# Kernel tuning notes

Measured on AMD Instinct MI355X. Metric: run time of the kernel, lower is better.

The kernel has to match this reference:

```python
import jax, jax.numpy as jnp
import numpy as np

N_NODES = 100000
N_EDGES = 3200000
N_GRAPHS = 512
F_IN = 128
HID = 256
N_LABELS = 10


def setup_inputs() -> dict:
    key = jax.random.key(0)
    ks = jax.random.split(key, 16)
    x = jax.random.normal(ks[0], (N_NODES, F_IN), dtype=jnp.float32)
    edge_index = jax.random.randint(ks[1], (2, N_EDGES), 0, N_NODES)
    batch = jnp.sort(jax.random.randint(ks[2], (N_NODES,), 0, N_GRAPHS))
    dims = [(F_IN, HID), (HID, HID), (HID, HID), (HID, HID // 2), (HID // 2, HID // 2), (HID // 2, HID // 4)]
    inp = {"x": x, "edge_index": edge_index, "batch": batch, "primary_idxs_in_batch": 0}
    for i, (di, do) in enumerate(dims, 1):
        inp[f"W{i}"] = jax.random.normal(ks[2 + i], (di, do), dtype=jnp.float32) * (1.0 / np.sqrt(di))
        inp[f"b{i}"] = jnp.zeros((do,), dtype=jnp.float32)
    inp["Wlin"] = jax.random.normal(ks[12], (HID // 4, N_LABELS), dtype=jnp.float32) * (1.0 / np.sqrt(HID // 4))
    inp["blin"] = jnp.zeros((N_LABELS,), dtype=jnp.float32)
    return inp


def _gcn_conv(h, W, b, src, dst, norm):
    # dense transform first (smaller of the two sides), then normalized scatter-aggregate
    m = (h @ W)[src] * norm[:, None]  # [E+N, C_out]
    return jax.ops.segment_sum(m, dst, num_segments=N_NODES) + b


def reference(x, edge_index, batch, primary_idxs_in_batch,
              W1, b1, W2, b2, W3, b3, W4, b4, W5, b5, W6, b6, Wlin, blin):
    loops = jnp.arange(N_NODES, dtype=edge_index.dtype)
    src = jnp.concatenate([edge_index[0], loops])  # A + I (self loops)
    dst = jnp.concatenate([edge_index[1], loops])
    deg = jax.ops.segment_sum(jnp.ones_like(dst, dtype=x.dtype), dst, num_segments=N_NODES)
    dinv = jnp.where(deg > 0, jax.lax.rsqrt(deg), 0.0)
    norm = dinv[src] * dinv[dst]  # D^-1/2 (A+I) D^-1/2 edge weights

    h = jax.nn.relu(_gcn_conv(x, W1, b1, src, dst, norm))
    h = jax.nn.relu(_gcn_conv(h, W2, b2, src, dst, norm))
    h = jax.nn.relu(_gcn_conv(h, W3, b3, src, dst, norm))
    h = jax.nn.relu(_gcn_conv(h, W4, b4, src, dst, norm))
    h = jax.nn.relu(_gcn_conv(h, W5, b5, src, dst, norm))
    h = _gcn_conv(h, W6, b6, src, dst, norm)

    # primary_idxs_in_batch is falsy (0) -> global_mean_pool path
    s = jax.ops.segment_sum(h, batch, num_segments=N_GRAPHS)
    cnt = jax.ops.segment_sum(jnp.ones((N_NODES,), dtype=h.dtype), batch, num_segments=N_GRAPHS)
    pooled = s / jnp.maximum(cnt, 1.0)[:, None]  # [G, HID//4]

    logits = pooled @ Wlin + blin  # [G, labels]
    return (jax.nn.log_softmax(logits, axis=1), jax.nn.softmax(logits, axis=1))
```

## Files before the change

kernel.cpp:

```cpp
#include <hip/hip_runtime.h>
#include <math.h>

#define NN 100000
#define NE 3200000
#define NG 512
#define NBK 782
#define EBLK 196
#define SBE 16384
#define STSH 13
#define NTIL 13

typedef __attribute__((ext_vector_type(8))) short short8;
typedef __attribute__((ext_vector_type(4))) float f32x4;
typedef __attribute__((ext_vector_type(2))) float f32x2;

__device__ __forceinline__ float bf2f(unsigned short h){
  return __uint_as_float(((unsigned int)h) << 16);
}
__device__ __forceinline__ unsigned short f2bf(float f){
  unsigned int u = __float_as_uint(f);
  unsigned int r = (u + 0x7fffu + ((u >> 16) & 1u)) >> 16;
  return (unsigned short)r;
}
__device__ __forceinline__ unsigned char f2fp8(float v){
  int p = __builtin_amdgcn_cvt_pk_fp8_f32(v, v, 0, 0);
  return (unsigned char)p;
}

__global__ __launch_bounds__(256) void hist2_k(const int* __restrict__ ei,
    int* __restrict__ cnt, int* __restrict__ btot){
  __shared__ int lh[NBK];
  int t = threadIdx.x, b = blockIdx.x;
  for (int i=t; i<NBK; i+=256) lh[i] = 0;
  __syncthreads();
  int base = b*SBE;
  #pragma unroll 8
  for (int u=0; u<SBE/256; u++){
    int e = base + u*256 + t;
    if (e < NE) atomicAdd(&lh[ei[NE + e] >> 7], 1);
  }
  __syncthreads();
  for (int i=t; i<NBK; i+=256){
    int v = lh[i];
    cnt[b*NBK + i] = v;
    if (v) atomicAdd(&btot[i], v);
  }
}
__global__ void bscan2_k(const int* __restrict__ btot, int* __restrict__ bptr){
  __shared__ int sc[1024];
  int t = threadIdx.x;
  int v = (t < NBK) ? btot[t] : 0;
  sc[t] = v; __syncthreads();
  for (int off=1; off<1024; off<<=1){
    int u = (t>=off) ? sc[t-off] : 0;
    __syncthreads(); sc[t] += u; __syncthreads();
  }
  if (t < NBK) bptr[t] = sc[t] - v;
  if (t == 1023) bptr[NBK] = sc[1023];
}
__global__ __launch_bounds__(256) void bkpfx_k(int* __restrict__ cnt, const int* __restrict__ bptr){
  __shared__ int sc[256];
  int b = blockIdx.x, t = threadIdx.x;
  int v = (t < EBLK) ? cnt[t*NBK + b] : 0;
  sc[t] = v; __syncthreads();
  for (int off=1; off<256; off<<=1){
    int u = (t>=off) ? sc[t-off] : 0;
    __syncthreads(); sc[t] += u; __syncthreads();
  }
  if (t < EBLK) cnt[t*NBK + b] = bptr[b] + sc[t] - v;
}
__global__ __launch_bounds__(256) void scat2_k(const int* __restrict__ ei,
    const int* __restrict__ cnt, unsigned int* __restrict__ ebuf){
  __shared__ int lh[NBK];
  __shared__ int lo[NBK];
  int t = threadIdx.x, b = blockIdx.x;
  for (int i=t; i<NBK; i+=256){ lh[i] = 0; lo[i] = cnt[b*NBK + i]; }
  __syncthreads();
  int base = b*SBE;
  #pragma unroll 8
  for (int u=0; u<SBE/256; u++){
    int e = base + u*256 + t;
    if (e < NE){
      int s = ei[e], d = ei[NE + e];
      int bk = d >> 7;
      int r = atomicAdd(&lh[bk], 1);
      ebuf[lo[bk] + r] = (unsigned)s | ((unsigned)(d & 127) << 17);
    }
  }
}
__global__ __launch_bounds__(256) void bcsr_k(const unsigned int* __restrict__ ebuf,
    const int* __restrict__ bptr, int* __restrict__ rp, float* __restrict__ dinv,
    int* __restrict__ col, int* __restrict__ permg){
  __shared__ int cnt2[128*NTIL];
  __shared__ int sc[128];
  __shared__ int dg[128];
  int b = blockIdx.x, t = threadIdx.x;
  int nbase = b << 7;
  int beg = bptr[b], end = bptr[b+1];
  for (int i = t; i < 128*NTIL; i += 256) cnt2[i] = 0;
  __syncthreads();
  for (int e = beg + t; e < end; e += 256){
    unsigned int sd = ebuf[e];
    int li = sd >> 17;
    int tile = (int)(sd & 0x1FFFFu) >> STSH;
    atomicAdd(&cnt2[li*NTIL + tile], 1);
  }
  __syncthreads();
  int v = 0;
  if (t < 128){
    #pragma unroll
    for (int k=0;k<NTIL;k++) v += cnt2[t*NTIL+k];
    sc[t] = v;
    dg[t] = ((nbase + t) < NN) ? v : 0x7FFFFFFF;
  }
  __syncthreads();
  for (int o2=1; o2<128; o2<<=1){
    int u = (t < 128 && t >= o2) ? sc[t-o2] : 0;
    __syncthreads();
    if (t < 128) sc[t] += u;
    __syncthreads();
  }
  if (t < 128){
    int node = nbase + t;
    int ex = beg + sc[t] - v;
    if (node < NN){
      rp[node] = ex;
      dinv[node] = rsqrtf((float)(v + 1));
    }
    int s = ex;
    #pragma unroll
    for (int k=0;k<NTIL;k++){
      int c = cnt2[t*NTIL+k];
      cnt2[t*NTIL+k] = s;
      s += c;
    }
    int d = dg[t];
    int rk = 0;
    #pragma unroll 4
    for (int u2=0; u2<128; u2++){
      int du = dg[u2];
      rk += (int)((du < d) || (du == d && u2 < t));
    }
    permg[nbase + rk] = node;
  }
  if (b == ((NN-1) >> 7) && t == 0) rp[NN] = end;
  __syncthreads();
  for (int e = beg + t; e < end; e += 256){
    unsigned int sd = ebuf[e];
    int li = sd >> 17;
    int src = (int)(sd & 0x1FFFF);
    int tile = src >> STSH;
    int pos = atomicAdd(&cnt2[li*NTIL + tile], 1);
    col[pos] = src;
  }
}

__global__ void f2q_k(const float* __restrict__ in, unsigned char* __restrict__ out, int n4){
  int i = blockIdx.x*256 + threadIdx.x;
  if (i < n4){
    float4 v = ((const float4*)in)[i];
    int p = __builtin_amdgcn_cvt_pk_fp8_f32(v.x, v.y, 0, 0);
    p = __builtin_amdgcn_cvt_pk_fp8_f32(v.z, v.w, p, 1);
    ((unsigned int*)out)[i] = (unsigned int)p;
  }
}
__global__ void wswz_all_k(const float* W1, const float* W2, const float* W3,
                           const float* W4, const float* W5, const float* W6,
                           unsigned short* O1, unsigned short* O2, unsigned short* O3,
                           unsigned short* O4, unsigned short* O5, unsigned short* O6){
  int cfg = blockIdx.y;
  int K, N; const float* W; unsigned short* out;
  switch(cfg){
    case 0: K=128; N=256; W=W1; out=O1; break;
    case 1: K=256; N=256; W=W2; out=O2; break;
    case 2: K=256; N=256; W=W3; out=O3; break;
    case 3: K=256; N=128; W=W4; out=O4; break;
    case 4: K=128; N=128; W=W5; out=O5; break;
    default:K=128; N=64;  W=W6; out=O6; break;
  }
  int idx = blockIdx.x*256 + threadIdx.x;
  int total = K*N/8;
  if (idx >= total) return;
  int l = idx & 15;
  int t = idx >> 4; int q = t & 3; t >>= 2;
  int NT = N/16;
  int nt = t % NT, kt = t / NT;
  int kbase = kt*32 + q*8, n = nt*16 + l;
  short8 o;
  #pragma unroll
  for (int j=0;j<8;j++) o[j] = (short)f2bf(W[(size_t)(kbase+j)*N + n]);
  *(short8*)(out + (size_t)idx*8) = o;
}

template<int RS, int W, bool SRC_SCALE, bool RELU, bool HAS_BIAS>
__global__ __launch_bounds__(256) void spmm8_k(const unsigned char* __restrict__ in,
    unsigned short* __restrict__ out,
    const int* __restrict__ rp, const int* __restrict__ col,
    const float* __restrict__ dinv, const int* __restrict__ perm,
    const float* __restrict__ bias)
{
  constexpr int LPR = W/16;
  constexpr int RPW = 64/LPR;
  constexpr int GP  = 128/RPW;
  int tid = threadIdx.x;
  int wv = tid >> 6, lane = tid & 63;
  int sub = lane / LPR, li = lane % LPR;
  int G = blockIdx.x*4 + wv;
  int bucket = G % NBK;
  int rg = (GP-1) - (G / NBK);
  int row = perm[(bucket << 7) + rg*RPW + sub];
  if (row >= NN) return;
  int beg = rp[row], end = rp[row+1];
  float di = dinv[row];
  int co = blockIdx.y*W + li*16;
  const unsigned char* inb = in + co;
  f32x2 acc2[8];
  {
    uint4 sv = *(const uint4*)(inb + (size_t)row*RS);
    acc2[0] = __builtin_amdgcn_cvt_pk_f32_fp8(sv.x, 0);
    acc2[1] = __builtin_amdgcn_cvt_pk_f32_fp8(sv.x, 1);
    acc2[2] = __builtin_amdgcn_cvt_pk_f32_fp8(sv.y, 0);
    acc2[3] = __builtin_amdgcn_cvt_pk_f32_fp8(sv.y, 1);
    acc2[4] = __builtin_amdgcn_cvt_pk_f32_fp8(sv.z, 0);
    acc2[5] = __builtin_amdgcn_cvt_pk_f32_fp8(sv.z, 1);
    acc2[6] = __builtin_amdgcn_cvt_pk_f32_fp8(sv.w, 0);
    acc2[7] = __builtin_amdgcn_cvt_pk_f32_fp8(sv.w, 1);
    if (SRC_SCALE){
      f32x2 d2 = (f32x2){di, di};
      #pragma unroll
      for (int k=0;k<8;k++) acc2[k] = acc2[k] * d2;
    }
  }
  int j = beg;
  for (; j+8 <= end; j += 8){
    int s[8]; uint4 v[8]; float wgt[8];
    #pragma unroll
    for (int u=0;u<8;u++) s[u] = col[j+u];
    #pragma unroll
    for (int u=0;u<8;u++) v[u] = *(const uint4*)(inb + (size_t)s[u]*RS);
    if (SRC_SCALE){
      #pragma unroll
      for (int u=0;u<8;u++) wgt[u] = dinv[s[u]];
    }
    #pragma unroll
    for (int u=0;u<8;u++){
      float w = SRC_SCALE ? wgt[u] : 1.f;
      f32x2 w2 = (f32x2){w, w};
      acc2[0] = __builtin_elementwise_fma(w2, __builtin_amdgcn_cvt_pk_f32_fp8(v[u].x, 0), acc2[0]);
      acc2[1] = __builtin_elementwise_fma(w2, __builtin_amdgcn_cvt_pk_f32_fp8(v[u].x, 1), acc2[1]);
      acc2[2] = __builtin_elementwise_fma(w2, __builtin_amdgcn_cvt_pk_f32_fp8(v[u].y, 0), acc2[2]);
      acc2[3] = __builtin_elementwise_fma(w2, __builtin_amdgcn_cvt_pk_f32_fp8(v[u].y, 1), acc2[3]);
      acc2[4] = __builtin_elementwise_fma(w2, __builtin_amdgcn_cvt_pk_f32_fp8(v[u].z, 0), acc2[4]);
      acc2[5] = __builtin_elementwise_fma(w2, __builtin_amdgcn_cvt_pk_f32_fp8(v[u].z, 1), acc2[5]);
      acc2[6] = __builtin_elementwise_fma(w2, __builtin_amdgcn_cvt_pk_f32_fp8(v[u].w, 0), acc2[6]);
      acc2[7] = __builtin_elementwise_fma(w2, __builtin_amdgcn_cvt_pk_f32_fp8(v[u].w, 1), acc2[7]);
    }
  }
  for (; j < end; j++){
    int ss = col[j];
    uint4 v = *(const uint4*)(inb + (size_t)ss*RS);
    float w = SRC_SCALE ? dinv[ss] : 1.f;
    f32x2 w2 = (f32x2){w, w};
    acc2[0] = __builtin_elementwise_fma(w2, __builtin_amdgcn_cvt_pk_f32_fp8(v.x, 0), acc2[0]);
    acc2[1] = __builtin_elementwise_fma(w2, __builtin_amdgcn_cvt_pk_f32_fp8(v.x, 1), acc2[1]);
    acc2[2] = __builtin_elementwise_fma(w2, __builtin_amdgcn_cvt_pk_f32_fp8(v.y, 0), acc2[2]);
    acc2[3] = __builtin_elementwise_fma(w2, __builtin_amdgcn_cvt_pk_f32_fp8(v.y, 1), acc2[3]);
    acc2[4] = __builtin_elementwise_fma(w2, __builtin_amdgcn_cvt_pk_f32_fp8(v.z, 0), acc2[4]);
    acc2[5] = __builtin_elementwise_fma(w2, __builtin_amdgcn_cvt_pk_f32_fp8(v.z, 1), acc2[5]);
    acc2[6] = __builtin_elementwise_fma(w2, __builtin_amdgcn_cvt_pk_f32_fp8(v.w, 0), acc2[6]);
    acc2[7] = __builtin_elementwise_fma(w2, __builtin_amdgcn_cvt_pk_f32_fp8(v.w, 1), acc2[7]);
  }
  float acc[16];
  #pragma unroll
  for (int k=0;k<8;k++){ acc[2*k] = acc2[k][0]; acc[2*k+1] = acc2[k][1]; }
  float bb[16];
  if (HAS_BIAS){
    #pragma unroll
    for (int u=0;u<4;u++) *(float4*)&bb[u*4] = *(const float4*)(bias + co + u*4);
  }
  #pragma unroll
  for (int v=0;v<16;v++){
    acc[v] *= di;
    if (HAS_BIAS) acc[v] += bb[v];
    if (RELU) acc[v] = fmaxf(acc[v], 0.f);
  }
  uint4 o0, o1;
  o0.x = (unsigned int)f2bf(acc[0])  | ((unsigned int)f2bf(acc[1])<<16);
  o0.y = (unsigned int)f2bf(acc[2])  | ((unsigned int)f2bf(acc[3])<<16);
  o0.z = (unsigned int)f2bf(acc[4])  | ((unsigned int)f2bf(acc[5])<<16);
  o0.w = (unsigned int)f2bf(acc[6])  | ((unsigned int)f2bf(acc[7])<<16);
  o1.x = (unsigned int)f2bf(acc[8])  | ((unsigned int)f2bf(acc[9])<<16);
  o1.y = (unsigned int)f2bf(acc[10]) | ((unsigned int)f2bf(acc[11])<<16);
  o1.z = (unsigned int)f2bf(acc[12]) | ((unsigned int)f2bf(acc[13])<<16);
  o1.w = (unsigned int)f2bf(acc[14]) | ((unsigned int)f2bf(acc[15])<<16);
  unsigned short* op = out + (size_t)row*RS + co;
  *(uint4*)op = o0;
  *(uint4*)(op + 8) = o1;
}

template<int K, int N, int EPI>
__global__ __launch_bounds__(256) void mgemm_k(const unsigned short* __restrict__ A,
    const unsigned short* __restrict__ Bsw,
    const float* __restrict__ aux, unsigned short* __restrict__ Cb,
    unsigned char* __restrict__ Cq, int M)
{
  constexpr int NT = 4;
  constexpr int KT = K/32;
  constexpr int NTF = N/16;
  __shared__ short8 Bl[KT*NT*64];
  int tid = threadIdx.x;
  int w = tid >> 6, lane = tid & 63;
  int l = lane & 15, q = lane >> 4;
  int nb0 = blockIdx.x * 64;
  int rb = blockIdx.y*256 + w*64;
  {
    const short8* bsrc = (const short8*)Bsw;
    for (int i = tid; i < KT*NT*64; i += 256){
      int kt = i >> 8;
      int rem = i & 255;
      Bl[i] = bsrc[(kt*NTF + (nb0 >> 4))*64 + rem];
    }
  }
  const unsigned short* ap[4];
  #pragma unroll
  for (int rt=0; rt<4; rt++){
    int r = min(rb + rt*16 + l, M-1);
    ap[rt] = A + (size_t)r*K + q*8;
  }
  f32x4 acc[4][NT];
  #pragma unroll
  for (int rt=0; rt<4; rt++)
    #pragma unroll
    for (int nt=0; nt<NT; nt++) acc[rt][nt] = (f32x4){0,0,0,0};
  short8 a[4], an[4];
  #pragma unroll
  for (int rt=0; rt<4; rt++) a[rt] = *(const short8*)(ap[rt]);
  __syncthreads();
  for (int kt=0; kt<KT; kt++){
    if (kt+1 < KT){
      #pragma unroll
      for (int rt=0; rt<4; rt++) an[rt] = *(const short8*)(ap[rt] + (kt+1)*32);
    }
    const short8* bl = &Bl[kt << 8];
    #pragma unroll
    for (int nt=0; nt<NT; nt++){
      short8 bf = bl[nt*64 + q*16 + l];
      acc[0][nt] = __builtin_amdgcn_mfma_f32_16x16x32_bf16(a[0], bf, acc[0][nt], 0,0,0);
      acc[1][nt] = __builtin_amdgcn_mfma_f32_16x16x32_bf16(a[1], bf, acc[1][nt], 0,0,0);
      acc[2][nt] = __builtin_amdgcn_mfma_f32_16x16x32_bf16(a[2], bf, acc[2][nt], 0,0,0);
      acc[3][nt] = __builtin_amdgcn_mfma_f32_16x16x32_bf16(a[3], bf, acc[3][nt], 0,0,0);
    }
    #pragma unroll
    for (int rt=0; rt<4; rt++) a[rt] = an[rt];
  }
  #pragma unroll
  for (int rt=0; rt<4; rt++){
    int rbb = rb + rt*16;
    #pragma unroll
    for (int nt=0; nt<NT; nt++){
      f32x4 av = acc[rt][nt];
      int n = nb0 + nt*16 + l;
      #pragma unroll
      for (int r=0;r<4;r++){
        int row = rbb + q*4 + r;
        if (row < M){
          float v = av[r];
          if (EPI == 0){
            v = fmaxf(v + aux[n], 0.f);
            Cb[(size_t)row*N + n] = f2bf(v);
          } else {
            v *= aux[row];
            Cq[(size_t)row*N + n] = f2fp8(v);
          }
        }
      }
    }
  }
}

__global__ __launch_bounds__(256) void poolhead_k(const unsigned short* __restrict__ h,
    const int* __restrict__ batch, const float* __restrict__ Wlin,
    const float* __restrict__ blin, float* __restrict__ out)
{
  __shared__ int range[2];
  __shared__ float red[4][64];
  __shared__ float pl[64];
  int g = blockIdx.x;
  if (threadIdx.x < 2){
    int target = g + threadIdx.x;
    int lo = 0, hi = NN;
    while (lo < hi){ int m = (lo+hi) >> 1; if (batch[m] < target) lo = m+1; else hi = m; }
    range[threadIdx.x] = lo;
  }
  __syncthreads();
  int lo = range[0], hi = range[1];
  int ch = threadIdx.x & 63, rg = threadIdx.x >> 6;
  float s = 0.f;
  for (int r = lo + rg; r < hi; r += 4) s += bf2f(h[(size_t)r*64 + ch]);
  red[rg][ch] = s; __syncthreads();
  if (rg == 0){
    float tot = red[0][ch] + red[1][ch] + red[2][ch] + red[3][ch];
    pl[ch] = tot / fmaxf((float)(hi - lo), 1.f);
  }
  __syncthreads();
  if (threadIdx.x == 0){
    float l[10];
    #pragma unroll
    for (int j=0;j<10;j++) l[j] = blin[j];
    for (int c=0;c<64;c++){
      float p = pl[c];
      #pragma unroll
      for (int j=0;j<10;j++) l[j] = fmaf(p, Wlin[c*10 + j], l[j]);
    }
    float mx = l[0];
    #pragma unroll
    for (int j=1;j<10;j++) mx = fmaxf(mx, l[j]);
    float e[10]; float se = 0.f;
    #pragma unroll
    for (int j=0;j<10;j++){ e[j] = expf(l[j]-mx); se += e[j]; }
    float lse = logf(se);
    #pragma unroll
    for (int j=0;j<10;j++){
      out[g*10 + j]         = l[j] - mx - lse;
      out[NG*10 + g*10 + j] = e[j] / se;
    }
  }
}

extern "C" void kernel_launch(void* const* d_in, const int* in_sizes, int n_in,
                              void* d_out, int out_size, void* d_ws, size_t ws_size,
                              hipStream_t stream)
{
  const float* x     = (const float*)d_in[0];
  const int*   ei    = (const int*)  d_in[1];
  const int*   batch = (const int*)  d_in[2];
  const float* W1=(const float*)d_in[4],  *b1=(const float*)d_in[5];
  const float* W2=(const float*)d_in[6],  *b2=(const float*)d_in[7];
  const float* W3=(const float*)d_in[8],  *b3=(const float*)d_in[9];
  const float* W4=(const float*)d_in[10], *b4=(const float*)d_in[11];
  const float* W5=(const float*)d_in[12], *b5=(const float*)d_in[13];
  const float* W6=(const float*)d_in[14], *b6=(const float*)d_in[15];
  const float* Wl=(const float*)d_in[16], *bl=(const float*)d_in[17];
  float* out = (float*)d_out;

  char* ws = (char*)d_ws;
  unsigned short* hA  = (unsigned short*)(ws + 0);
  unsigned short* hB  = (unsigned short*)(ws + 51200000);
  unsigned char*  hQ  = (unsigned char*) (ws + 102400000);
  unsigned char*  xq  = (unsigned char*) (ws + 128000000);
  int*   col   = (int*)  (ws + 140800000);
  unsigned int* ebuf = (unsigned int*)(ws + 153600000);
  int*   rp    = (int*)  (ws + 166400000);
  float* dinv  = (float*)(ws + 166800016);
  unsigned short* W1s = (unsigned short*)(ws + 167200016);
  unsigned short* W2s = (unsigned short*)(ws + 167265552);
  unsigned short* W3s = (unsigned short*)(ws + 167396624);
  unsigned short* W4s = (unsigned short*)(ws + 167527696);
  unsigned short* W5s = (unsigned short*)(ws + 167593232);
  unsigned short* W6s = (unsigned short*)(ws + 167626000);
  int*   btot  = (int*)  (ws + 167642896);
  int*   bptr  = (int*)  (ws + 167646032);
  int*   cnt   = (int*)  (ws + 167649184);
  int*   perm  = cnt;

  hipMemsetAsync(btot, 0, NBK*4, stream);

  hist2_k <<<EBLK, 256, 0, stream>>>(ei, cnt, btot);
  bscan2_k<<<1, 1024, 0, stream>>>(btot, bptr);
  bkpfx_k <<<NBK, 256, 0, stream>>>(cnt, bptr);
  scat2_k <<<EBLK, 256, 0, stream>>>(ei, cnt, ebuf);
  bcsr_k  <<<NBK, 256, 0, stream>>>(ebuf, bptr, rp, dinv, col, perm);

  wswz_all_k<<<dim3(32,6), 256, 0, stream>>>(W1,W2,W3,W4,W5,W6, W1s,W2s,W3s,W4s,W5s,W6s);
  f2q_k<<<(NN*128/4 + 255)/256, 256, 0, stream>>>(x, xq, NN*128/4);

  const int GX128 = NBK*16/4;
  const int GX64  = NBK*8/4;
  const int GX    = (NN + 255)/256;

  spmm8_k<128,128,true,false,false><<<dim3(GX128,1),256,0,stream>>>(xq, hA, rp, col, dinv, perm, nullptr);
  mgemm_k<128,256,0><<<dim3(4,GX),256,0,stream>>>(hA, W1s, b1, hB, nullptr, NN);
  mgemm_k<256,256,1><<<dim3(4,GX),256,0,stream>>>(hB, W2s, dinv, nullptr, hQ, NN);
  spmm8_k<256,128,false,true,true><<<dim3(GX128,2),256,0,stream>>>(hQ, hA, rp, col, dinv, perm, b2);
  mgemm_k<256,256,1><<<dim3(4,GX),256,0,stream>>>(hA, W3s, dinv, nullptr, hQ, NN);
  spmm8_k<256,128,false,true,true><<<dim3(GX128,2),256,0,stream>>>(hQ, hB, rp, col, dinv, perm, b3);
  mgemm_k<256,128,1><<<dim3(2,GX),256,0,stream>>>(hB, W4s, dinv, nullptr, hQ, NN);
  spmm8_k<128,128,false,true,true><<<dim3(GX128,1),256,0,stream>>>(hQ, hA, rp, col, dinv, perm, b4);
  mgemm_k<128,128,1><<<dim3(2,GX),256,0,stream>>>(hA, W5s, dinv, nullptr, hQ, NN);
  spmm8_k<128,128,false,true,true><<<dim3(GX128,1),256,0,stream>>>(hQ, hB, rp, col, dinv, perm, b5);
  mgemm_k<128,64,1><<<dim3(1,GX),256,0,stream>>>(hB, W6s, dinv, nullptr, hQ, NN);
  spmm8_k<64,64,false,false,true><<<dim3(GX64,1),256,0,stream>>>(hQ, hA, rp, col, dinv, perm, b6);

  poolhead_k<<<NG, 256, 0, stream>>>(hA, batch, Wl, bl, out);
}
```

Measured before the change: 1.017 ms.

## Merge preprocessing kernels and remap GEMM blocks for XCD-local reuse

Combines the histogram, weight swizzle and fp8 input quantization into one launch, and folds the single-block bucket scan into the per-bucket prefix kernel, where each block recomputes its own prefix with a reduction. This removes several kernel launches and serialization points. The GEMM grid becomes 1D and is remapped so that consecutive row tiles land on the same XCD while sharing column slices, aiming to improve L2 reuse of the A rows. The added cost is a redundant partial sum over btot in every bkpfx block and some out-of-range blocks that return early.

```diff
diff --git a/kernel.cpp b/kernel.cpp
--- a/kernel.cpp
+++ b/kernel.cpp
@@ -9,6 +9,9 @@
 #define SBE 16384
 #define STSH 13
 #define NTIL 13
+#define HB 196
+#define WB 192
+#define QB 12500
 
 typedef __attribute__((ext_vector_type(8))) short short8;
 typedef __attribute__((ext_vector_type(4))) float f32x4;
@@ -27,47 +30,92 @@
   return (unsigned char)p;
 }
 
-__global__ __launch_bounds__(256) void hist2_k(const int* __restrict__ ei,
-    int* __restrict__ cnt, int* __restrict__ btot){
+__global__ __launch_bounds__(256) void pre_k(const int* __restrict__ ei,
+    int* __restrict__ cnt, int* __restrict__ btot,
+    const float* __restrict__ x, unsigned char* __restrict__ xq,
+    const float* W1, const float* W2, const float* W3,
+    const float* W4, const float* W5, const float* W6,
+    unsigned short* O1, unsigned short* O2, unsigned short* O3,
+    unsigned short* O4, unsigned short* O5, unsigned short* O6)
+{
   __shared__ int lh[NBK];
-  int t = threadIdx.x, b = blockIdx.x;
-  for (int i=t; i<NBK; i+=256) lh[i] = 0;
-  __syncthreads();
-  int base = b*SBE;
-  #pragma unroll 8
-  for (int u=0; u<SBE/256; u++){
-    int e = base + u*256 + t;
-    if (e < NE) atomicAdd(&lh[ei[NE + e] >> 7], 1);
-  }
-  __syncthreads();
-  for (int i=t; i<NBK; i+=256){
-    int v = lh[i];
-    cnt[b*NBK + i] = v;
-    if (v) atomicAdd(&btot[i], v);
-  }
-}
-__global__ void bscan2_k(const int* __restrict__ btot, int* __restrict__ bptr){
-  __shared__ int sc[1024];
-  int t = threadIdx.x;
-  int v = (t < NBK) ? btot[t] : 0;
-  sc[t] = v; __syncthreads();
-  for (int off=1; off<1024; off<<=1){
-    int u = (t>=off) ? sc[t-off] : 0;
-    __syncthreads(); sc[t] += u; __syncthreads();
-  }
-  if (t < NBK) bptr[t] = sc[t] - v;
-  if (t == 1023) bptr[NBK] = sc[1023];
-}
-__global__ __launch_bounds__(256) void bkpfx_k(int* __restrict__ cnt, const int* __restrict__ bptr){
+  int b = blockIdx.x, t = threadIdx.x;
+  if (b < HB){
+    for (int i=t; i<NBK; i+=256) lh[i] = 0;
+    __syncthreads();
+    int base = b*SBE;
+    #pragma unroll 8
+    for (int u=0; u<SBE/256; u++){
+      int e = base + u*256 + t;
+      if (e < NE) atomicAdd(&lh[ei[NE + e] >> 7], 1);
+    }
+    __syncthreads();
+    for (int i=t; i<NBK; i+=256){
+      int v = lh[i];
+      cnt[b*NBK + i] = v;
+      if (v) atomicAdd(&btot[i], v);
+    }
+    return;
+  }
+  if (b < HB + WB){
+    int bb = b - HB;
+    int cfg = bb >> 5, bx = bb & 31;
+    int K, N; const float* W; unsigned short* out;
+    switch(cfg){
+      case 0: K=128; N=256; W=W1; out=O1; break;
+      case 1: K=256; N=256; W=W2; out=O2; break;
+      case 2: K=256; N=256; W=W3; out=O3; break;
+      case 3: K=256; N=128; W=W4; out=O4; break;
+      case 4: K=128; N=128; W=W5; out=O5; break;
+      default:K=128; N=64;  W=W6; out=O6; break;
+    }
+    int idx = bx*256 + t;
+    int total = K*N/8;
+    if (idx >= total) return;
+    int l = idx & 15;
+    int tt = idx >> 4; int q = tt & 3; tt >>= 2;
+    int NT = N/16;
+    int nt = tt % NT, kt = tt / NT;
+    int kbase = kt*32 + q*8, n = nt*16 + l;
+    short8 o;
+    #pragma unroll
+    for (int j=0;j<8;j++) o[j] = (short)f2bf(W[(size_t)(kbase+j)*N + n]);
+    *(short8*)(out + (size_t)idx*8) = o;
+    return;
+  }
+  {
+    int i = (b - HB - WB)*256 + t;
+    float4 v = ((const float4*)x)[i];
+    int p = __builtin_amdgcn_cvt_pk_fp8_f32(v.x, v.y, 0, 0);
+    p = __builtin_amdgcn_cvt_pk_fp8_f32(v.z, v.w, p, 1);
+    ((unsigned int*)xq)[i] = (unsigned int)p;
+  }
+}
+
+__global__ __launch_bounds__(256) void bkpfx_k(int* __restrict__ cnt,
+    const int* __restrict__ btot, int* __restrict__ bptr){
   __shared__ int sc[256];
   int b = blockIdx.x, t = threadIdx.x;
+  int p = 0;
+  for (int i = t; i < b; i += 256) p += btot[i];
+  sc[t] = p; __syncthreads();
+  for (int off=128; off>0; off>>=1){
+    if (t < off) sc[t] += sc[t+off];
+    __syncthreads();
+  }
+  int pb = sc[0];
+  __syncthreads();
+  if (t == 0){
+    bptr[b] = pb;
+    if (b == NBK-1) bptr[NBK] = pb + btot[b];
+  }
   int v = (t < EBLK) ? cnt[t*NBK + b] : 0;
   sc[t] = v; __syncthreads();
   for (int off=1; off<256; off<<=1){
     int u = (t>=off) ? sc[t-off] : 0;
     __syncthreads(); sc[t] += u; __syncthreads();
   }
-  if (t < EBLK) cnt[t*NBK + b] = bptr[b] + sc[t] - v;
+  if (t < EBLK) cnt[t*NBK + b] = pb + sc[t] - v;
 }
 __global__ __launch_bounds__(256) void scat2_k(const int* __restrict__ ei,
     const int* __restrict__ cnt, unsigned int* __restrict__ ebuf){
@@ -153,43 +201,6 @@
     int pos = atomicAdd(&cnt2[li*NTIL + tile], 1);
     col[pos] = src;
   }
-}
-
-__global__ void f2q_k(const float* __restrict__ in, unsigned char* __restrict__ out, int n4){
-  int i = blockIdx.x*256 + threadIdx.x;
-  if (i < n4){
-    float4 v = ((const float4*)in)[i];
-    int p = __builtin_amdgcn_cvt_pk_fp8_f32(v.x, v.y, 0, 0);
-    p = __builtin_amdgcn_cvt_pk_fp8_f32(v.z, v.w, p, 1);
-    ((unsigned int*)out)[i] = (unsigned int)p;
-  }
-}
-__global__ void wswz_all_k(const float* W1, const float* W2, const float* W3,
-                           const float* W4, const float* W5, const float* W6,
-                           unsigned short* O1, unsigned short* O2, unsigned short* O3,
-                           unsigned short* O4, unsigned short* O5, unsigned short* O6){
-  int cfg = blockIdx.y;
-  int K, N; const float* W; unsigned short* out;
-  switch(cfg){
-    case 0: K=128; N=256; W=W1; out=O1; break;
-    case 1: K=256; N=256; W=W2; out=O2; break;
-    case 2: K=256; N=256; W=W3; out=O3; break;
-    case 3: K=256; N=128; W=W4; out=O4; break;
-    case 4: K=128; N=128; W=W5; out=O5; break;
-    default:K=128; N=64;  W=W6; out=O6; break;
-  }
-  int idx = blockIdx.x*256 + threadIdx.x;
-  int total = K*N/8;
-  if (idx >= total) return;
-  int l = idx & 15;
-  int t = idx >> 4; int q = t & 3; t >>= 2;
-  int NT = N/16;
-  int nt = t % NT, kt = t / NT;
-  int kbase = kt*32 + q*8, n = nt*16 + l;
-  short8 o;
-  #pragma unroll
-  for (int j=0;j<8;j++) o[j] = (short)f2bf(W[(size_t)(kbase+j)*N + n]);
-  *(short8*)(out + (size_t)idx*8) = o;
 }
 
 template<int RS, int W, bool SRC_SCALE, bool RELU, bool HAS_BIAS>
@@ -307,12 +318,18 @@
   constexpr int NT = 4;
   constexpr int KT = K/32;
   constexpr int NTF = N/16;
+  constexpr int NSL = N/64;
   __shared__ short8 Bl[KT*NT*64];
   int tid = threadIdx.x;
   int w = tid >> 6, lane = tid & 63;
   int l = lane & 15, q = lane >> 4;
-  int nb0 = blockIdx.x * 64;
-  int rb = blockIdx.y*256 + w*64;
+  int id = blockIdx.x;
+  int xcd = id & 7, s = id >> 3;
+  int xsl = s % NSL;
+  int y = (s / NSL)*8 + xcd;
+  if (y >= (M + 255)/256) return;
+  int nb0 = xsl * 64;
+  int rb = y*256 + w*64;
   {
     const short8* bsrc = (const short8*)Bsw;
     for (int i = tid; i < KT*NT*64; i += 256){
@@ -465,30 +482,31 @@
 
   hipMemsetAsync(btot, 0, NBK*4, stream);
 
-  hist2_k <<<EBLK, 256, 0, stream>>>(ei, cnt, btot);
-  bscan2_k<<<1, 1024, 0, stream>>>(btot, bptr);
-  bkpfx_k <<<NBK, 256, 0, stream>>>(cnt, bptr);
+  pre_k <<<HB+WB+QB, 256, 0, stream>>>(ei, cnt, btot, x, xq,
+      W1,W2,W3,W4,W5,W6, W1s,W2s,W3s,W4s,W5s,W6s);
+  bkpfx_k <<<NBK, 256, 0, stream>>>(cnt, btot, bptr);
   scat2_k <<<EBLK, 256, 0, stream>>>(ei, cnt, ebuf);
   bcsr_k  <<<NBK, 256, 0, stream>>>(ebuf, bptr, rp, dinv, col, perm);
 
-  wswz_all_k<<<dim3(32,6), 256, 0, stream>>>(W1,W2,W3,W4,W5,W6, W1s,W2s,W3s,W4s,W5s,W6s);
-  f2q_k<<<(NN*128/4 + 255)/256, 256, 0, stream>>>(x, xq, NN*128/4);
-
   const int GX128 = NBK*16/4;
   const int GX64  = NBK*8/4;
-  const int GX    = (NN + 255)/256;
+  const int GT    = (NN + 255)/256;
+  const int GY8   = (GT + 7)/8;
+  const int G256  = 8*4*GY8;
+  const int G128  = 8*2*GY8;
+  const int G64   = 8*1*GY8;
 
   spmm8_k<128,128,true,false,false><<<dim3(GX128,1),256,0,stream>>>(xq, hA, rp, col, dinv, perm, nullptr);
-  mgemm_k<128,256,0><<<dim3(4,GX),256,0,stream>>>(hA, W1s, b1, hB, nullptr, NN);
-  mgemm_k<256,256,1><<<dim3(4,GX),256,0,stream>>>(hB, W2s, dinv, nullptr, hQ, NN);
+  mgemm_k<128,256,0><<<G256,256,0,stream>>>(hA, W1s, b1, hB, nullptr, NN);
+  mgemm_k<256,256,1><<<G256,256,0,stream>>>(hB, W2s, dinv, nullptr, hQ, NN);
   spmm8_k<256,128,false,true,true><<<dim3(GX128,2),256,0,stream>>>(hQ, hA, rp, col, dinv, perm, b2);
-  mgemm_k<256,256,1><<<dim3(4,GX),256,0,stream>>>(hA, W3s, dinv, nullptr, hQ, NN);
+  mgemm_k<256,256,1><<<G256,256,0,stream>>>(hA, W3s, dinv, nullptr, hQ, NN);
   spmm8_k<256,128,false,true,true><<<dim3(GX128,2),256,0,stream>>>(hQ, hB, rp, col, dinv, perm, b3);
-  mgemm_k<256,128,1><<<dim3(2,GX),256,0,stream>>>(hB, W4s, dinv, nullptr, hQ, NN);
+  mgemm_k<256,128,1><<<G128,256,0,stream>>>(hB, W4s, dinv, nullptr, hQ, NN);
   spmm8_k<128,128,false,true,true><<<dim3(GX128,1),256,0,stream>>>(hQ, hA, rp, col, dinv, perm, b4);
-  mgemm_k<128,128,1><<<dim3(2,GX),256,0,stream>>>(hA, W5s, dinv, nullptr, hQ, NN);
+  mgemm_k<128,128,1><<<G128,256,0,stream>>>(hA, W5s, dinv, nullptr, hQ, NN);
   spmm8_k<128,128,false,true,true><<<dim3(GX128,1),256,0,stream>>>(hQ, hB, rp, col, dinv, perm, b5);
-  mgemm_k<128,64,1><<<dim3(1,GX),256,0,stream>>>(hB, W6s, dinv, nullptr, hQ, NN);
+  mgemm_k<128,64,1><<<G64,256,0,stream>>>(hB, W6s, dinv, nullptr, hQ, NN);
   spmm8_k<64,64,false,false,true><<<dim3(GX64,1),256,0,stream>>>(hQ, hA, rp, col, dinv, perm, b6);
 
   poolhead_k<<<NG, 256, 0, stream>>>(hA, batch, Wl, bl, out);
```

Result: faster. 962.7 us (-5.3%).
